# Kernel optimization log

Measured on AMD Instinct MI355X. Metric: run time of the kernel, lower is better.

The kernel has to match this reference:

```python
import jax, jax.numpy as jnp
import numpy as np

LEAKY_SLOPE = 0.01

def bilinear_interpolate(grid, coords):
    # grid: [H, W, C]; coords: [N, 2] in [0,1] (x, y order as in torch code)
    H = grid.shape[0] - 1
    W = grid.shape[1] - 1
    fx = coords[:, 0] * W
    fy = coords[:, 1] * H
    x0 = fx.astype(jnp.int32)
    y0 = fy.astype(jnp.int32)
    xf = jnp.mod(fx, 1.0)
    yf = jnp.mod(fy, 1.0)
    x1 = jnp.minimum(x0 + 1, W)
    y1 = jnp.minimum(y0 + 1, H)
    tl = grid[y0, x0]  # [N, C]
    tr = grid[y0, x1]
    bl = grid[y1, x0]
    br = grid[y1, x1]
    xf = xf[:, None]
    yf = yf[:, None]
    top = (1.0 - xf) * tl + xf * tr
    bot = (1.0 - xf) * bl + xf * br
    return (1.0 - yf) * top + yf * bot


def setup_inputs() -> dict:
    key = jax.random.key(0)
    ks = jax.random.split(key, 10)
    N = 2097152
    pos = jax.random.uniform(ks[0], (N, 2), dtype=jnp.float32)
    dir = jax.random.uniform(ks[1], (N, 2), dtype=jnp.float32)
    pos_grid = jax.random.normal(ks[2], (256, 256, 3), dtype=jnp.float32) * 10.0
    dir_grid = jax.random.normal(ks[3], (256, 256, 3), dtype=jnp.float32) * 10.0
    # Linear layers: PyTorch default init U(-1/sqrt(fan_in), 1/sqrt(fan_in))
    def linear(kw, kb, fan_in, fan_out):
        bound = 1.0 / np.sqrt(fan_in)
        W = jax.random.uniform(kw, (fan_out, fan_in), minval=-bound, maxval=bound, dtype=jnp.float32)
        b = jax.random.uniform(kb, (fan_out,), minval=-bound, maxval=bound, dtype=jnp.float32)
        return W, b
    W1, b1 = linear(ks[4], ks[5], 6, 64)
    W2, b2 = linear(ks[6], ks[7], 64, 64)
    W3, b3 = linear(ks[8], ks[9], 64, 1)
    return {"pos": pos, "dir": dir, "pos_grid": pos_grid, "dir_grid": dir_grid,
            "W1": W1, "b1": b1, "W2": W2, "b2": b2, "W3": W3, "b3": b3}


def reference(pos, dir, pos_grid, dir_grid, W1, b1, W2, b2, W3, b3):
    pos_feat = jax.lax.stop_gradient(bilinear_interpolate(pos_grid, pos))  # .detach() in torch
    dir_feat = jax.lax.stop_gradient(bilinear_interpolate(dir_grid, dir))
    x = jnp.concatenate([pos_feat, dir_feat], axis=1)  # [N, 6]
    x = jax.nn.leaky_relu(x @ W1.T + b1, LEAKY_SLOPE)
    x = jax.nn.leaky_relu(x @ W2.T + b2, LEAKY_SLOPE)
    return jax.nn.sigmoid(x @ W3.T + b3)  # [N, 1]
```

## Files before the change

### kernel.cpp

```cpp
#include <hip/hip_runtime.h>
#include <hip/hip_bf16.h>
#include <math.h>


#define NTHREADS 256
#define NB 4
#define LSTRIDE 72
#define WAVE_LDS (64 * LSTRIDE)

typedef __attribute__((ext_vector_type(8))) short bf16x8;
typedef __attribute__((ext_vector_type(4))) float f32x4;
typedef __attribute__((ext_vector_type(4))) int i32x4;
typedef __attribute__((ext_vector_type(2))) int i32x2;

static __device__ __forceinline__ short f2bf(float f) {
    return __builtin_bit_cast(short, __float2bfloat16(f));
}
static __device__ __forceinline__ int pk2(float lo, float hi) {
    unsigned short l = (unsigned short)f2bf(lo);
    unsigned short h = (unsigned short)f2bf(hi);
    return (int)(((unsigned int)h << 16) | (unsigned int)l);
}

static __device__ __forceinline__ void bilerp3(const float* __restrict__ g,
                                               float px, float py, float* f) {
    float fx = px * 255.0f;
    float fy = py * 255.0f;
    int x0 = (int)fx;
    int y0 = (int)fy;
    float xf = fx - floorf(fx);
    float yf = fy - floorf(fy);
    int x1 = min(x0 + 1, 255);
    int y1 = min(y0 + 1, 255);
    const float* r00 = g + (y0 * 256 + x0) * 3;
    const float* r01 = g + (y0 * 256 + x1) * 3;
    const float* r10 = g + (y1 * 256 + x0) * 3;
    const float* r11 = g + (y1 * 256 + x1) * 3;
#pragma unroll
    for (int ch = 0; ch < 3; ++ch) {
        float tl = r00[ch], tr = r01[ch], bl = r10[ch], br = r11[ch];
        float top = fmaf(xf, tr - tl, tl);
        float bot = fmaf(xf, br - bl, bl);
        f[ch] = fmaf(yf, bot - top, top);
    }
}

__global__ __launch_bounds__(NTHREADS, 3) void mlp_mfma_kernel(
    const float* __restrict__ pos, const float* __restrict__ dir,
    const float* __restrict__ pos_grid, const float* __restrict__ dir_grid,
    const float* __restrict__ W1, const float* __restrict__ b1,
    const float* __restrict__ W2, const float* __restrict__ b2,
    const float* __restrict__ W3, const float* __restrict__ b3,
    float* __restrict__ out) {
    __shared__ short lds_all[4 * WAVE_LDS];

    const int w = threadIdx.x >> 6;
    const int lane = threadIdx.x & 63;
    const int c = lane & 15;
    const int q = lane >> 4;

    short* L = lds_all + w * WAVE_LDS;

    bf16x8 A1f[4];
#pragma unroll
    for (int mt = 0; mt < 4; ++mt) {
        int f = mt * 16 + c;
        bf16x8 t;
#pragma unroll
        for (int j = 0; j < 8; ++j) {
            float v = 0.0f;
            if (q == 0) {
                if (j < 6) v = W1[f * 6 + j];
                else if (j == 6) v = b1[f];
            }
            t[j] = f2bf(v);
        }
        A1f[mt] = t;
    }
    bf16x8 A2f[2][4];
#pragma unroll
    for (int kt = 0; kt < 2; ++kt)
#pragma unroll
        for (int mt = 0; mt < 4; ++mt) {
            int n2 = mt * 16 + c;
            int k0 = kt * 32 + q * 8;
            bf16x8 t;
#pragma unroll
            for (int j = 0; j < 8; ++j) t[j] = f2bf(W2[n2 * 64 + k0 + j]);
            A2f[kt][mt] = t;
        }
    f32x4 ci[4], w3q[4];
#pragma unroll
    for (int ft = 0; ft < 4; ++ft)
#pragma unroll
        for (int r = 0; r < 4; ++r) {
            ci[ft][r] = b2[ft * 16 + q * 4 + r];
            w3q[ft][r] = W3[ft * 16 + q * 4 + r];
        }
    const float b3s = b3[0];

    const long wave_global = (long)blockIdx.x * 4 + w;
    const long base0 = wave_global * (64L * NB);
    const f32x4 zacc = {0.f, 0.f, 0.f, 0.f};

    float2 pp = ((const float2*)pos)[base0 + lane];
    float2 dd = ((const float2*)dir)[base0 + lane];

#pragma unroll 1
    for (int ib = 0; ib < NB; ++ib) {
        const long base = base0 + ib * 64;
        const long nbase = (ib + 1 < NB) ? (base + 64) : base;
        float2 ppn = ((const float2*)pos)[nbase + lane];
        float2 ddn = ((const float2*)dir)[nbase + lane];

        float feat[6];
        bilerp3(pos_grid, pp.x, pp.y, feat);
        bilerp3(dir_grid, dd.x, dd.y, feat + 3);
        int d0 = pk2(feat[0], feat[1]);
        int d1 = pk2(feat[2], feat[3]);
        int d2 = pk2(feat[4], feat[5]);
        int d3 = pk2(1.0f, 0.0f);

        float s[4];
#pragma unroll
        for (int pt = 0; pt < 4; ++pt) {
            const int row = pt * 16 + c;
            const int addr = row << 2;
            i32x4 bi;
            bi[0] = __builtin_amdgcn_ds_bpermute(addr, d0);
            bi[1] = __builtin_amdgcn_ds_bpermute(addr, d1);
            bi[2] = __builtin_amdgcn_ds_bpermute(addr, d2);
            bi[3] = __builtin_amdgcn_ds_bpermute(addr, d3);
            bf16x8 bfrag = __builtin_bit_cast(bf16x8, bi);

            f32x4 a1[4];
#pragma unroll
            for (int mt = 0; mt < 4; ++mt)
                a1[mt] = __builtin_amdgcn_mfma_f32_16x16x32_bf16(
                    A1f[mt], bfrag, zacc, 0, 0, 0);

#pragma unroll
            for (int mt = 0; mt < 4; ++mt) {
                float l0 = a1[mt][0], l1 = a1[mt][1];
                float l2 = a1[mt][2], l3 = a1[mt][3];
                l0 = fmaxf(l0, 0.01f * l0);
                l1 = fmaxf(l1, 0.01f * l1);
                l2 = fmaxf(l2, 0.01f * l2);
                l3 = fmaxf(l3, 0.01f * l3);
                i32x2 wv;
                wv[0] = pk2(l0, l1);
                wv[1] = pk2(l2, l3);
                *(i32x2*)(L + row * LSTRIDE + mt * 16 + q * 4) = wv;
            }

            bf16x8 h0 = *(const bf16x8*)(L + row * LSTRIDE + q * 8);
            bf16x8 h1 = *(const bf16x8*)(L + row * LSTRIDE + 32 + q * 8);

            f32x4 a2[4];
#pragma unroll
            for (int ft = 0; ft < 4; ++ft) a2[ft] = ci[ft];
#pragma unroll
            for (int ft = 0; ft < 4; ++ft) {
                a2[ft] = __builtin_amdgcn_mfma_f32_16x16x32_bf16(
                    A2f[0][ft], h0, a2[ft], 0, 0, 0);
                a2[ft] = __builtin_amdgcn_mfma_f32_16x16x32_bf16(
                    A2f[1][ft], h1, a2[ft], 0, 0, 0);
            }

            float t = 0.0f;
#pragma unroll
            for (int ft = 0; ft < 4; ++ft)
#pragma unroll
                for (int r = 0; r < 4; ++r) {
                    float x = a2[ft][r];
                    x = fmaxf(x, 0.01f * x);
                    t = fmaf(x, w3q[ft][r], t);
                }
            t += __shfl_xor(t, 16, 64);
            t += __shfl_xor(t, 32, 64);
            s[pt] = t;
        }

        float sa = (q & 1) ? s[1] : s[0];
        float sb = (q & 1) ? s[3] : s[2];
        float v = (q & 2) ? sb : sa;
        v += b3s;
        v = 1.0f / (1.0f + __expf(-v));
        out[base + q * 16 + c] = v;

        pp = ppn;
        dd = ddn;
    }
}

extern "C" void kernel_launch(void* const* d_in, const int* in_sizes, int n_in,
                              void* d_out, int out_size, void* d_ws,
                              size_t ws_size, hipStream_t stream) {
    const float* pos = (const float*)d_in[0];
    const float* dir = (const float*)d_in[1];
    const float* pos_grid = (const float*)d_in[2];
    const float* dir_grid = (const float*)d_in[3];
    const float* W1 = (const float*)d_in[4];
    const float* b1 = (const float*)d_in[5];
    const float* W2 = (const float*)d_in[6];
    const float* b2 = (const float*)d_in[7];
    const float* W3 = (const float*)d_in[8];
    const float* b3 = (const float*)d_in[9];
    float* out = (float*)d_out;

    const int n = in_sizes[0] / 2;
    const int batches = n / 64;
    const int waves = batches / NB;
    const int blocks = waves / 4;

    mlp_mfma_kernel<<<blocks, NTHREADS, 0, stream>>>(
        pos, dir, pos_grid, dir_grid, W1, b1, W2, b2, W3, b3, out);
}
```

Measured before the change: 158.7 us.

## Software-pipeline bilinear gathers into double-buffered LDS and split MLP layers

Precomputes the interpolated features for the next batch between the layer-1 and layer-2 MFMA phases and stores them in a double-buffered per-wave LDS buffer. Layer 1 now reads its B fragments straight from LDS instead of using four ds_bpermute shuffles per tile. The goal is to hide the latency of the grid gather loads behind layer-2 MFMA work. Layer 2 is also restructured to chain the two MFMAs per feature tile and reduce immediately, which lowers register pressure. The cost is extra LDS usage, which may affect occupancy, plus one redundant gather on the last iteration.

```diff
diff --git a/kernel.cpp b/kernel.cpp
--- a/kernel.cpp
+++ b/kernel.cpp
@@ -6,7 +6,7 @@
 #define NTHREADS 256
 #define NB 4
 #define LSTRIDE 72
-#define WAVE_LDS (64 * LSTRIDE)
+#define WAVE_L (64 * LSTRIDE)
 
 typedef __attribute__((ext_vector_type(8))) short bf16x8;
 typedef __attribute__((ext_vector_type(4))) float f32x4;
@@ -52,14 +52,16 @@
     const float* __restrict__ W2, const float* __restrict__ b2,
     const float* __restrict__ W3, const float* __restrict__ b3,
     float* __restrict__ out) {
-    __shared__ short lds_all[4 * WAVE_LDS];
+    __shared__ short lds_L[4 * WAVE_L];
+    __shared__ int lds_F[4 * 2 * 64 * 4];
 
     const int w = threadIdx.x >> 6;
     const int lane = threadIdx.x & 63;
     const int c = lane & 15;
     const int q = lane >> 4;
 
-    short* L = lds_all + w * WAVE_LDS;
+    short* L = lds_L + w * WAVE_L;
+    int* FB = lds_F + w * (2 * 64 * 4);
 
     bf16x8 A1f[4];
 #pragma unroll
@@ -98,47 +100,41 @@
             w3q[ft][r] = W3[ft * 16 + q * 4 + r];
         }
     const float b3s = b3[0];
+    const int dbias = pk2(1.0f, 0.0f);
 
     const long wave_global = (long)blockIdx.x * 4 + w;
     const long base0 = wave_global * (64L * NB);
     const f32x4 zacc = {0.f, 0.f, 0.f, 0.f};
 
-    float2 pp = ((const float2*)pos)[base0 + lane];
-    float2 dd = ((const float2*)dir)[base0 + lane];
+    {
+        float2 pp = ((const float2*)pos)[base0 + lane];
+        float2 dd = ((const float2*)dir)[base0 + lane];
+        float feat[6];
+        bilerp3(pos_grid, pp.x, pp.y, feat);
+        bilerp3(dir_grid, dd.x, dd.y, feat + 3);
+        i32x4 dv;
+        dv[0] = pk2(feat[0], feat[1]);
+        dv[1] = pk2(feat[2], feat[3]);
+        dv[2] = pk2(feat[4], feat[5]);
+        dv[3] = dbias;
+        *(i32x4*)(FB + lane * 4) = dv;
+    }
 
 #pragma unroll 1
     for (int ib = 0; ib < NB; ++ib) {
         const long base = base0 + ib * 64;
-        const long nbase = (ib + 1 < NB) ? (base + 64) : base;
-        float2 ppn = ((const float2*)pos)[nbase + lane];
-        float2 ddn = ((const float2*)dir)[nbase + lane];
-
-        float feat[6];
-        bilerp3(pos_grid, pp.x, pp.y, feat);
-        bilerp3(dir_grid, dd.x, dd.y, feat + 3);
-        int d0 = pk2(feat[0], feat[1]);
-        int d1 = pk2(feat[2], feat[3]);
-        int d2 = pk2(feat[4], feat[5]);
-        int d3 = pk2(1.0f, 0.0f);
-
-        float s[4];
+        const int cur = ib & 1;
+
 #pragma unroll
         for (int pt = 0; pt < 4; ++pt) {
             const int row = pt * 16 + c;
-            const int addr = row << 2;
-            i32x4 bi;
-            bi[0] = __builtin_amdgcn_ds_bpermute(addr, d0);
-            bi[1] = __builtin_amdgcn_ds_bpermute(addr, d1);
-            bi[2] = __builtin_amdgcn_ds_bpermute(addr, d2);
-            bi[3] = __builtin_amdgcn_ds_bpermute(addr, d3);
+            i32x4 bi = *(const i32x4*)(FB + cur * 256 + row * 4);
             bf16x8 bfrag = __builtin_bit_cast(bf16x8, bi);
-
             f32x4 a1[4];
 #pragma unroll
             for (int mt = 0; mt < 4; ++mt)
                 a1[mt] = __builtin_amdgcn_mfma_f32_16x16x32_bf16(
                     A1f[mt], bfrag, zacc, 0, 0, 0);
-
 #pragma unroll
             for (int mt = 0; mt < 4; ++mt) {
                 float l0 = a1[mt][0], l1 = a1[mt][1];
@@ -152,30 +148,43 @@
                 wv[1] = pk2(l2, l3);
                 *(i32x2*)(L + row * LSTRIDE + mt * 16 + q * 4) = wv;
             }
-
+        }
+
+        {
+            const long nbase = (ib + 1 < NB) ? (base + 64) : base;
+            float2 pp = ((const float2*)pos)[nbase + lane];
+            float2 dd = ((const float2*)dir)[nbase + lane];
+            float feat[6];
+            bilerp3(pos_grid, pp.x, pp.y, feat);
+            bilerp3(dir_grid, dd.x, dd.y, feat + 3);
+            i32x4 dv;
+            dv[0] = pk2(feat[0], feat[1]);
+            dv[1] = pk2(feat[2], feat[3]);
+            dv[2] = pk2(feat[4], feat[5]);
+            dv[3] = dbias;
+            *(i32x4*)(FB + (cur ^ 1) * 256 + lane * 4) = dv;
+        }
+
+        float s[4];
+#pragma unroll
+        for (int pt = 0; pt < 4; ++pt) {
+            const int row = pt * 16 + c;
             bf16x8 h0 = *(const bf16x8*)(L + row * LSTRIDE + q * 8);
             bf16x8 h1 = *(const bf16x8*)(L + row * LSTRIDE + 32 + q * 8);
-
-            f32x4 a2[4];
-#pragma unroll
-            for (int ft = 0; ft < 4; ++ft) a2[ft] = ci[ft];
+            float t = 0.0f;
 #pragma unroll
             for (int ft = 0; ft < 4; ++ft) {
-                a2[ft] = __builtin_amdgcn_mfma_f32_16x16x32_bf16(
-                    A2f[0][ft], h0, a2[ft], 0, 0, 0);
-                a2[ft] = __builtin_amdgcn_mfma_f32_16x16x32_bf16(
-                    A2f[1][ft], h1, a2[ft], 0, 0, 0);
-            }
-
-            float t = 0.0f;
-#pragma unroll
-            for (int ft = 0; ft < 4; ++ft)
+                f32x4 t0 = __builtin_amdgcn_mfma_f32_16x16x32_bf16(
+                    A2f[0][ft], h0, ci[ft], 0, 0, 0);
+                f32x4 a2 = __builtin_amdgcn_mfma_f32_16x16x32_bf16(
+                    A2f[1][ft], h1, t0, 0, 0, 0);
 #pragma unroll
                 for (int r = 0; r < 4; ++r) {
-                    float x = a2[ft][r];
+                    float x = a2[r];
                     x = fmaxf(x, 0.01f * x);
                     t = fmaf(x, w3q[ft][r], t);
                 }
+            }
             t += __shfl_xor(t, 16, 64);
             t += __shfl_xor(t, 32, 64);
             s[pt] = t;
@@ -187,9 +196,6 @@
         v += b3s;
         v = 1.0f / (1.0f + __expf(-v));
         out[base + q * 16 + c] = v;
-
-        pp = ppn;
-        dd = ddn;
     }
 }
 
```

Result: slower. 168.8 us (+6.3%).
